# Optimization experiments

Measured on AMD Instinct MI355X. Metric: run time of the kernel, lower is better.

The kernel has to match this reference:

```python
import jax, jax.numpy as jnp
import numpy as np

N, D, C = 32768, 1024, 256
GAMMA = 1e-4


def setup_inputs() -> dict:
    key = jax.random.key(0)
    kx, kw = jax.random.split(key)
    X = jax.random.normal(kx, (N, D), dtype=jnp.float32)
    # lcls linear params: weight [C, D], bias [C] (torch nn.Linear layout)
    W = jax.random.normal(kw, (C, D), dtype=jnp.float32) * (1.0 / np.sqrt(D))
    b = jnp.zeros((C,), dtype=jnp.float32)
    return {"X": X, "W": W, "b": b}


def reference(X, W, b):
    # P = softmax(X @ W.T + b) over cluster dim C
    P = jax.nn.softmax(X @ W.T + b, axis=-1)            # [N, C]
    # Reorder P @ P.T @ X -> P @ (P.T @ X): avoids the O(N^2) affinity matrix
    PtX = jnp.einsum('nc,nd->cd', P, X)                  # [C, D]
    return X + GAMMA * (P @ PtX)                         # [N, D]
```

## Files before the change

kernel.cpp:

```cpp
#include <hip/hip_runtime.h>
#include <hip/hip_bf16.h>
#include <stdint.h>

#define N_TOK 32768
#define DIM   1024
#define NC    256
#define GAMMA_F 1e-4f

typedef unsigned short u16;
typedef __attribute__((ext_vector_type(8))) short bf16x8;
typedef __attribute__((ext_vector_type(4))) float f32x4;

__device__ __forceinline__ u16 f2b(float f) {
  union { float f; uint32_t u; } c; c.f = f;
  uint32_t u = c.u;
  return (u16)((u + 0x7FFFu + ((u >> 16) & 1u)) >> 16);
}

__device__ __forceinline__ void gll16(const void* g, void* l) {
  __builtin_amdgcn_global_load_lds(
      (const __attribute__((address_space(1))) unsigned int*)g,
      (__attribute__((address_space(3))) unsigned int*)l, 16, 0, 0);
}

__global__ __launch_bounds__(256) void k0_transpose(const float* __restrict__ X,
                                                    u16* __restrict__ TX) {
  __shared__ u16 tile[64][68];
  const int n0 = blockIdx.x * 64;
  const int d0 = blockIdx.y * 64;
  const int t = threadIdx.x;
  const int r = t >> 4;
  const int c4 = (t & 15) * 4;
#pragma unroll
  for (int i = 0; i < 4; ++i) {
    const int row = r + i * 16;
    const float4 v = *reinterpret_cast<const float4*>(&X[(size_t)(n0 + row) * DIM + d0 + c4]);
    tile[row][c4 + 0] = f2b(v.x);
    tile[row][c4 + 1] = f2b(v.y);
    tile[row][c4 + 2] = f2b(v.z);
    tile[row][c4 + 3] = f2b(v.w);
  }
  __syncthreads();
#pragma unroll
  for (int i = 0; i < 4; ++i) {
    const int drow = r + i * 16;
    ushort4 o;
    o.x = tile[c4 + 0][drow];
    o.y = tile[c4 + 1][drow];
    o.z = tile[c4 + 2][drow];
    o.w = tile[c4 + 3][drow];
    *reinterpret_cast<ushort4*>(&TX[(size_t)(d0 + drow) * N_TOK + n0 + c4]) = o;
  }
}

__global__ __launch_bounds__(256) void k0_convert_w(const float* __restrict__ W,
                                                    u16* __restrict__ Wb) {
  const int idx = (blockIdx.x * 256 + threadIdx.x) * 4;
  const float4 v = *reinterpret_cast<const float4*>(&W[idx]);
  ushort4 o;
  o.x = f2b(v.x); o.y = f2b(v.y); o.z = f2b(v.z); o.w = f2b(v.w);
  *reinterpret_cast<ushort4*>(&Wb[idx]) = o;
}

__global__ __launch_bounds__(256, 3) void p1_gemm(const float* __restrict__ X,
                                                  const u16* __restrict__ Wb,
                                                  float* __restrict__ S) {
  __shared__ u16 As[128 * 64];
  __shared__ u16 Bs[128 * 64];
  const int t = threadIdx.x;
  const int lane = t & 63, wave = t >> 6;
  const int wm = wave & 1, wn = wave >> 1;
  const int n0 = blockIdx.x * 128;
  const int c0 = blockIdx.y * 128;
  const int frow = lane & 15, fk = (lane >> 4) * 8;
  const int sr = t >> 3, sc = (t & 7) * 8;
  const int laneoff = lane * 8;
  f32x4 acc[4][4] = {};
  for (int kt = 0; kt < 16; ++kt) {
    const int k0 = kt * 64;
#pragma unroll
    for (int p = 0; p < 4; ++p) {
      const int row = sr + p * 32;
      const float4 v0 = *reinterpret_cast<const float4*>(&X[(size_t)(n0 + row) * DIM + k0 + sc]);
      const float4 v1 = *reinterpret_cast<const float4*>(&X[(size_t)(n0 + row) * DIM + k0 + sc + 4]);
      bf16x8 u;
      u[0] = (short)f2b(v0.x); u[1] = (short)f2b(v0.y);
      u[2] = (short)f2b(v0.z); u[3] = (short)f2b(v0.w);
      u[4] = (short)f2b(v1.x); u[5] = (short)f2b(v1.y);
      u[6] = (short)f2b(v1.z); u[7] = (short)f2b(v1.w);
      *reinterpret_cast<bf16x8*>(&As[row * 64 + sc]) = u;
    }
#pragma unroll
    for (int i = 0; i < 4; ++i) {
      const int e = (wave * 4 + i) * 512;
      const int brow = (e + laneoff) >> 6;
      const int bcol = (e + laneoff) & 63;
      gll16(&Wb[(size_t)(c0 + brow) * DIM + k0 + bcol], &Bs[e]);
    }
    __syncthreads();
#pragma unroll
    for (int ks = 0; ks < 2; ++ks) {
      bf16x8 af[4], bg[4];
#pragma unroll
      for (int m = 0; m < 4; ++m)
        af[m] = *reinterpret_cast<const bf16x8*>(&As[(wm * 64 + m * 16 + frow) * 64 + ks * 32 + fk]);
#pragma unroll
      for (int n = 0; n < 4; ++n)
        bg[n] = *reinterpret_cast<const bf16x8*>(&Bs[(wn * 64 + n * 16 + frow) * 64 + ks * 32 + fk]);
#pragma unroll
      for (int m = 0; m < 4; ++m)
#pragma unroll
        for (int n = 0; n < 4; ++n)
          acc[m][n] = __builtin_amdgcn_mfma_f32_16x16x32_bf16(af[m], bg[n], acc[m][n], 0, 0, 0);
    }
    __syncthreads();
  }
#pragma unroll
  for (int m = 0; m < 4; ++m) {
    const int row = wm * 64 + m * 16 + (lane >> 4) * 4;
#pragma unroll
    for (int n = 0; n < 4; ++n) {
      const int col = wn * 64 + n * 16 + frow;
#pragma unroll
      for (int j = 0; j < 4; ++j)
        S[(size_t)(n0 + row + j) * NC + c0 + col] = acc[m][n][j];
    }
  }
}

__global__ __launch_bounds__(256) void k1_softmax(const float* __restrict__ S,
                                                  const float* __restrict__ bias,
                                                  u16* __restrict__ P,
                                                  u16* __restrict__ PT) {
  __shared__ u16 T[64][256];
  const int t = threadIdx.x;
  const int w = t >> 6, lane = t & 63;
  const int n0 = blockIdx.x * 64;
  const int col = lane * 4;
  const float4 bv = *reinterpret_cast<const float4*>(&bias[col]);
#pragma unroll
  for (int i = 0; i < 16; ++i) {
    const int row = i * 4 + w;
    float4 v = *reinterpret_cast<const float4*>(&S[(size_t)(n0 + row) * NC + col]);
    v.x += bv.x; v.y += bv.y; v.z += bv.z; v.w += bv.w;
    float mx = fmaxf(fmaxf(v.x, v.y), fmaxf(v.z, v.w));
    for (int s = 1; s < 64; s <<= 1) mx = fmaxf(mx, __shfl_xor(mx, s, 64));
    const float k = 1.44269504088896f;
    const float e0 = exp2f((v.x - mx) * k), e1 = exp2f((v.y - mx) * k);
    const float e2 = exp2f((v.z - mx) * k), e3 = exp2f((v.w - mx) * k);
    float sm = e0 + e1 + e2 + e3;
    for (int s = 1; s < 64; s <<= 1) sm += __shfl_xor(sm, s, 64);
    const float inv = 1.0f / sm;
    ushort4 o;
    o.x = f2b(e0 * inv); o.y = f2b(e1 * inv); o.z = f2b(e2 * inv); o.w = f2b(e3 * inv);
    *reinterpret_cast<ushort4*>(&P[(size_t)(n0 + row) * NC + col]) = o;
    *reinterpret_cast<ushort4*>(&T[row][col]) = o;
  }
  __syncthreads();
  const int c = t;
#pragma unroll
  for (int g = 0; g < 16; ++g) {
    ushort4 o;
    o.x = T[g * 4 + 0][c];
    o.y = T[g * 4 + 1][c];
    o.z = T[g * 4 + 2][c];
    o.w = T[g * 4 + 3][c];
    *reinterpret_cast<ushort4*>(&PT[(size_t)c * N_TOK + n0 + g * 4]) = o;
  }
}

__global__ __launch_bounds__(256, 3) void p2_gemm(const u16* __restrict__ TX,
                                                  const u16* __restrict__ PT,
                                                  float* __restrict__ part) {
  __shared__ u16 As[128 * 64];
  __shared__ u16 Bs[128 * 64];
  const int t = threadIdx.x;
  const int lane = t & 63, wave = t >> 6;
  const int wm = wave & 1, wn = wave >> 1;
  const int sk = blockIdx.x;
  const int d0 = (blockIdx.y >> 1) * 128;
  const int c0 = (blockIdx.y & 1) * 128;
  const int frow = lane & 15, fk = (lane >> 4) * 8;
  const int laneoff = lane * 8;
  f32x4 acc[4][4] = {};
  for (int kt = 0; kt < 16; ++kt) {
    const size_t k0 = (size_t)sk * 1024 + kt * 64;
#pragma unroll
    for (int i = 0; i < 4; ++i) {
      const int e = (wave * 4 + i) * 512;
      const int brow = (e + laneoff) >> 6;
      const int bcol = (e + laneoff) & 63;
      gll16(&TX[(size_t)(d0 + brow) * N_TOK + k0 + bcol], &As[e]);
      gll16(&PT[(size_t)(c0 + brow) * N_TOK + k0 + bcol], &Bs[e]);
    }
    __syncthreads();
#pragma unroll
    for (int ks = 0; ks < 2; ++ks) {
      bf16x8 af[4], bg[4];
#pragma unroll
      for (int m = 0; m < 4; ++m)
        af[m] = *reinterpret_cast<const bf16x8*>(&As[(wm * 64 + m * 16 + frow) * 64 + ks * 32 + fk]);
#pragma unroll
      for (int n = 0; n < 4; ++n)
        bg[n] = *reinterpret_cast<const bf16x8*>(&Bs[(wn * 64 + n * 16 + frow) * 64 + ks * 32 + fk]);
#pragma unroll
      for (int m = 0; m < 4; ++m)
#pragma unroll
        for (int n = 0; n < 4; ++n)
          acc[m][n] = __builtin_amdgcn_mfma_f32_16x16x32_bf16(af[m], bg[n], acc[m][n], 0, 0, 0);
    }
    __syncthreads();
  }
  float* pl = part + (size_t)sk * (DIM * NC);
#pragma unroll
  for (int m = 0; m < 4; ++m) {
    const int row = wm * 64 + m * 16 + (lane >> 4) * 4;
#pragma unroll
    for (int n = 0; n < 4; ++n) {
      const int colc = wn * 64 + n * 16 + frow;
#pragma unroll
      for (int j = 0; j < 4; ++j)
        pl[(size_t)(d0 + row + j) * NC + c0 + colc] = acc[m][n][j];
    }
  }
}

__global__ __launch_bounds__(256) void k2_reduce(const float* __restrict__ part,
                                                 u16* __restrict__ PtXb) {
  const int g = (blockIdx.x * 256 + threadIdx.x) * 4;
  f32x4 s = {0.f, 0.f, 0.f, 0.f};
#pragma unroll
  for (int p = 0; p < 32; ++p)
    s += *reinterpret_cast<const f32x4*>(&part[(size_t)p * (DIM * NC) + g]);
  ushort4 o;
  o.x = f2b(s[0] * GAMMA_F); o.y = f2b(s[1] * GAMMA_F);
  o.z = f2b(s[2] * GAMMA_F); o.w = f2b(s[3] * GAMMA_F);
  *reinterpret_cast<ushort4*>(&PtXb[g]) = o;
}

__global__ __launch_bounds__(256, 3) void p3_gemm(const u16* __restrict__ P,
                                                  const u16* __restrict__ PtXb,
                                                  const float* __restrict__ X,
                                                  float* __restrict__ Out) {
  __shared__ u16 As[128 * 64];
  __shared__ u16 Bs[128 * 64];
  const int t = threadIdx.x;
  const int lane = t & 63, wave = t >> 6;
  const int wm = wave & 1, wn = wave >> 1;
  const int n0 = blockIdx.x * 128;
  const int d0 = blockIdx.y * 128;
  const int frow = lane & 15, fk = (lane >> 4) * 8;
  const int laneoff = lane * 8;
  f32x4 acc[4][4] = {};
  for (int kt = 0; kt < 4; ++kt) {
    const int k0 = kt * 64;
#pragma unroll
    for (int i = 0; i < 4; ++i) {
      const int e = (wave * 4 + i) * 512;
      const int brow = (e + laneoff) >> 6;
      const int bcol = (e + laneoff) & 63;
      gll16(&P[(size_t)(n0 + brow) * NC + k0 + bcol], &As[e]);
      gll16(&PtXb[(size_t)(d0 + brow) * NC + k0 + bcol], &Bs[e]);
    }
    __syncthreads();
#pragma unroll
    for (int ks = 0; ks < 2; ++ks) {
      bf16x8 af[4], bg[4];
#pragma unroll
      for (int m = 0; m < 4; ++m)
        af[m] = *reinterpret_cast<const bf16x8*>(&As[(wm * 64 + m * 16 + frow) * 64 + ks * 32 + fk]);
#pragma unroll
      for (int n = 0; n < 4; ++n)
        bg[n] = *reinterpret_cast<const bf16x8*>(&Bs[(wn * 64 + n * 16 + frow) * 64 + ks * 32 + fk]);
#pragma unroll
      for (int m = 0; m < 4; ++m)
#pragma unroll
        for (int n = 0; n < 4; ++n)
          acc[m][n] = __builtin_amdgcn_mfma_f32_16x16x32_bf16(af[m], bg[n], acc[m][n], 0, 0, 0);
    }
    __syncthreads();
  }
#pragma unroll
  for (int m = 0; m < 4; ++m) {
    const int row = wm * 64 + m * 16 + (lane >> 4) * 4;
#pragma unroll
    for (int n = 0; n < 4; ++n) {
      const int colc = wn * 64 + n * 16 + frow;
#pragma unroll
      for (int j = 0; j < 4; ++j) {
        const size_t off = (size_t)(n0 + row + j) * DIM + d0 + colc;
        Out[off] = X[off] + acc[m][n][j];
      }
    }
  }
}

extern "C" void kernel_launch(void* const* d_in, const int* in_sizes, int n_in,
                              void* d_out, int out_size, void* d_ws, size_t ws_size,
                              hipStream_t stream) {
  const float* X = (const float*)d_in[0];
  const float* W = (const float*)d_in[1];
  const float* b = (const float*)d_in[2];
  float* Out = (float*)d_out;
  char* ws = (char*)d_ws;

  const size_t OFF_TX   = 0;
  const size_t OFF_WB   = (size_t)64 << 20;
  const size_t OFF_PTXB = OFF_WB + ((size_t)512 << 10);
  const size_t OFF_S    = (size_t)65 << 20;
  const size_t OFF_P    = (size_t)97 << 20;
  const size_t OFF_PT   = (size_t)113 << 20;
  const size_t NEED     = (size_t)129 << 20;
  if (ws_size < NEED) return;

  u16*   TX   = (u16*)(ws + OFF_TX);
  u16*   Wb   = (u16*)(ws + OFF_WB);
  u16*   PtXb = (u16*)(ws + OFF_PTXB);
  float* S    = (float*)(ws + OFF_S);
  float* part = S;
  u16*   Pp   = (u16*)(ws + OFF_P);
  u16*   PT   = (u16*)(ws + OFF_PT);

  k0_transpose<<<dim3(N_TOK / 64, DIM / 64), 256, 0, stream>>>(X, TX);
  k0_convert_w<<<dim3((NC * DIM) / 1024), 256, 0, stream>>>(W, Wb);
  p1_gemm<<<dim3(N_TOK / 128, NC / 128), 256, 0, stream>>>(X, Wb, S);
  k1_softmax<<<dim3(N_TOK / 64), 256, 0, stream>>>(S, b, Pp, PT);
  p2_gemm<<<dim3(32, 16), 256, 0, stream>>>(TX, PT, part);
  k2_reduce<<<dim3((DIM * NC) / 1024), 256, 0, stream>>>(part, PtXb);
  p3_gemm<<<dim3(N_TOK / 128, DIM / 128), 256, 0, stream>>>(Pp, PtXb, X, Out);
}
```

Before: 439.6 us.

## Fuse logits GEMM with softmax, swizzle LDS tiles, stage epilogues through LDS

The first GEMM and the softmax become one kernel. Each block now computes a full 64x256 logit tile, applies bias and softmax from shared memory, and writes P and its transpose directly. This removes the fp32 S round trip through global memory and one kernel launch. All three GEMMs also get XOR-swizzled LDS layouts to reduce bank conflicts. The p2 and p3 epilogues are staged through LDS so stores are coalesced float4 writes. The cost is a larger LDS footprint, with occupancy dropping from 3 to 2 blocks per CU.

```diff
diff --git a/kernel.cpp b/kernel.cpp
--- a/kernel.cpp
+++ b/kernel.cpp
@@ -22,6 +22,7 @@
       (const __attribute__((address_space(1))) unsigned int*)g,
       (__attribute__((address_space(3))) unsigned int*)l, 16, 0, 0);
 }
+
 
 __global__ __launch_bounds__(256) void k0_transpose(const float* __restrict__ X,
                                                     u16* __restrict__ TX) {
@@ -62,147 +63,158 @@
   *reinterpret_cast<ushort4*>(&Wb[idx]) = o;
 }
 
-__global__ __launch_bounds__(256, 3) void p1_gemm(const float* __restrict__ X,
-                                                  const u16* __restrict__ Wb,
-                                                  float* __restrict__ S) {
-  __shared__ u16 As[128 * 64];
-  __shared__ u16 Bs[128 * 64];
+__global__ __launch_bounds__(256, 2) void p1_fused(const float* __restrict__ X,
+                                                   const u16* __restrict__ Wb,
+                                                   const float* __restrict__ bias,
+                                                   u16* __restrict__ P,
+                                                   u16* __restrict__ PT) {
+  __shared__ __align__(16) char smem[66560];
+  u16* As = (u16*)smem;
+  u16* Bs = (u16*)(smem + 8192);
   const int t = threadIdx.x;
   const int lane = t & 63, wave = t >> 6;
   const int wm = wave & 1, wn = wave >> 1;
-  const int n0 = blockIdx.x * 128;
-  const int c0 = blockIdx.y * 128;
-  const int frow = lane & 15, fk = (lane >> 4) * 8;
-  const int sr = t >> 3, sc = (t & 7) * 8;
-  const int laneoff = lane * 8;
-  f32x4 acc[4][4] = {};
+  const int n0 = blockIdx.x * 64;
+  const int frow = lane & 15, fq = lane >> 4;
+  const int au = t & 7, ar0 = t >> 3;
+  const int bug = (lane & 7) ^ (lane >> 3);
+
+  f32x4 acc[2][8] = {};
   for (int kt = 0; kt < 16; ++kt) {
     const int k0 = kt * 64;
 #pragma unroll
-    for (int p = 0; p < 4; ++p) {
-      const int row = sr + p * 32;
-      const float4 v0 = *reinterpret_cast<const float4*>(&X[(size_t)(n0 + row) * DIM + k0 + sc]);
-      const float4 v1 = *reinterpret_cast<const float4*>(&X[(size_t)(n0 + row) * DIM + k0 + sc + 4]);
+    for (int h = 0; h < 2; ++h) {
+      const int r = ar0 + h * 32;
+      const size_t gb = (size_t)(n0 + r) * DIM + k0 + au * 8;
+      const float4 v0 = *reinterpret_cast<const float4*>(&X[gb]);
+      const float4 v1 = *reinterpret_cast<const float4*>(&X[gb + 4]);
       bf16x8 u;
       u[0] = (short)f2b(v0.x); u[1] = (short)f2b(v0.y);
       u[2] = (short)f2b(v0.z); u[3] = (short)f2b(v0.w);
       u[4] = (short)f2b(v1.x); u[5] = (short)f2b(v1.y);
       u[6] = (short)f2b(v1.z); u[7] = (short)f2b(v1.w);
-      *reinterpret_cast<bf16x8*>(&As[row * 64 + sc]) = u;
-    }
-#pragma unroll
-    for (int i = 0; i < 4; ++i) {
-      const int e = (wave * 4 + i) * 512;
-      const int brow = (e + laneoff) >> 6;
-      const int bcol = (e + laneoff) & 63;
-      gll16(&Wb[(size_t)(c0 + brow) * DIM + k0 + bcol], &Bs[e]);
+      *reinterpret_cast<bf16x8*>(&As[r * 64 + ((au ^ (r & 7)) * 8)]) = u;
+    }
+#pragma unroll
+    for (int i = 0; i < 8; ++i) {
+      const int chunk = wave * 8 + i;
+      const int brow = chunk * 8 + (lane >> 3);
+      gll16(&Wb[(size_t)brow * DIM + k0 + bug * 8], &Bs[chunk * 512]);
     }
     __syncthreads();
 #pragma unroll
     for (int ks = 0; ks < 2; ++ks) {
-      bf16x8 af[4], bg[4];
-#pragma unroll
-      for (int m = 0; m < 4; ++m)
-        af[m] = *reinterpret_cast<const bf16x8*>(&As[(wm * 64 + m * 16 + frow) * 64 + ks * 32 + fk]);
-#pragma unroll
-      for (int n = 0; n < 4; ++n)
-        bg[n] = *reinterpret_cast<const bf16x8*>(&Bs[(wn * 64 + n * 16 + frow) * 64 + ks * 32 + fk]);
-#pragma unroll
-      for (int m = 0; m < 4; ++m)
-#pragma unroll
-        for (int n = 0; n < 4; ++n)
+      bf16x8 af[2], bg[8];
+#pragma unroll
+      for (int m = 0; m < 2; ++m) {
+        const int r = wm * 32 + m * 16 + frow;
+        af[m] = *reinterpret_cast<const bf16x8*>(&As[r * 64 + (((ks * 4 + fq) ^ (r & 7)) * 8)]);
+      }
+#pragma unroll
+      for (int n = 0; n < 8; ++n) {
+        const int r = wn * 128 + n * 16 + frow;
+        bg[n] = *reinterpret_cast<const bf16x8*>(&Bs[r * 64 + (((ks * 4 + fq) ^ (r & 7)) * 8)]);
+      }
+#pragma unroll
+      for (int m = 0; m < 2; ++m)
+#pragma unroll
+        for (int n = 0; n < 8; ++n)
           acc[m][n] = __builtin_amdgcn_mfma_f32_16x16x32_bf16(af[m], bg[n], acc[m][n], 0, 0, 0);
     }
     __syncthreads();
   }
-#pragma unroll
-  for (int m = 0; m < 4; ++m) {
-    const int row = wm * 64 + m * 16 + (lane >> 4) * 4;
-#pragma unroll
-    for (int n = 0; n < 4; ++n) {
-      const int col = wn * 64 + n * 16 + frow;
+  float* Sf = (float*)smem;
+#pragma unroll
+  for (int m = 0; m < 2; ++m)
+#pragma unroll
+    for (int n = 0; n < 8; ++n) {
+      const int row = wm * 32 + m * 16 + fq * 4;
+      const int col = wn * 128 + n * 16 + frow;
 #pragma unroll
       for (int j = 0; j < 4; ++j)
-        S[(size_t)(n0 + row + j) * NC + c0 + col] = acc[m][n][j];
-    }
-  }
-}
-
-__global__ __launch_bounds__(256) void k1_softmax(const float* __restrict__ S,
-                                                  const float* __restrict__ bias,
-                                                  u16* __restrict__ P,
-                                                  u16* __restrict__ PT) {
-  __shared__ u16 T[64][256];
-  const int t = threadIdx.x;
-  const int w = t >> 6, lane = t & 63;
-  const int n0 = blockIdx.x * 64;
-  const int col = lane * 4;
-  const float4 bv = *reinterpret_cast<const float4*>(&bias[col]);
+        Sf[(row + j) * 260 + col] = acc[m][n][j];
+    }
+  __syncthreads();
+  u16* Su = (u16*)smem;
+  const float4 bv = *reinterpret_cast<const float4*>(&bias[lane * 4]);
+  const float l2e = 1.44269504088896f;
 #pragma unroll
   for (int i = 0; i < 16; ++i) {
-    const int row = i * 4 + w;
-    float4 v = *reinterpret_cast<const float4*>(&S[(size_t)(n0 + row) * NC + col]);
+    const int row = wave * 16 + i;
+    float4 v = *reinterpret_cast<const float4*>(&Sf[row * 260 + lane * 4]);
     v.x += bv.x; v.y += bv.y; v.z += bv.z; v.w += bv.w;
     float mx = fmaxf(fmaxf(v.x, v.y), fmaxf(v.z, v.w));
+#pragma unroll
     for (int s = 1; s < 64; s <<= 1) mx = fmaxf(mx, __shfl_xor(mx, s, 64));
-    const float k = 1.44269504088896f;
-    const float e0 = exp2f((v.x - mx) * k), e1 = exp2f((v.y - mx) * k);
-    const float e2 = exp2f((v.z - mx) * k), e3 = exp2f((v.w - mx) * k);
+    const float e0 = exp2f((v.x - mx) * l2e), e1 = exp2f((v.y - mx) * l2e);
+    const float e2 = exp2f((v.z - mx) * l2e), e3 = exp2f((v.w - mx) * l2e);
     float sm = e0 + e1 + e2 + e3;
+#pragma unroll
     for (int s = 1; s < 64; s <<= 1) sm += __shfl_xor(sm, s, 64);
     const float inv = 1.0f / sm;
     ushort4 o;
-    o.x = f2b(e0 * inv); o.y = f2b(e1 * inv); o.z = f2b(e2 * inv); o.w = f2b(e3 * inv);
-    *reinterpret_cast<ushort4*>(&P[(size_t)(n0 + row) * NC + col]) = o;
-    *reinterpret_cast<ushort4*>(&T[row][col]) = o;
-  }
-  __syncthreads();
-  const int c = t;
-#pragma unroll
-  for (int g = 0; g < 16; ++g) {
+    o.x = f2b(e0 * inv); o.y = f2b(e1 * inv);
+    o.z = f2b(e2 * inv); o.w = f2b(e3 * inv);
+    *reinterpret_cast<ushort4*>(&P[(size_t)(n0 + row) * NC + lane * 4]) = o;
+    const int rb = row & 31;
+    Su[row * 520 + (((lane * 4 + 0) ^ rb)) * 2] = o.x;
+    Su[row * 520 + (((lane * 4 + 1) ^ rb)) * 2] = o.y;
+    Su[row * 520 + (((lane * 4 + 2) ^ rb)) * 2] = o.z;
+    Su[row * 520 + (((lane * 4 + 3) ^ rb)) * 2] = o.w;
+  }
+  __syncthreads();
+#pragma unroll
+  for (int it = 0; it < 16; ++it) {
+    const int c = it * 16 + wave * 4 + fq;
+    const int n = frow * 4;
     ushort4 o;
-    o.x = T[g * 4 + 0][c];
-    o.y = T[g * 4 + 1][c];
-    o.z = T[g * 4 + 2][c];
-    o.w = T[g * 4 + 3][c];
-    *reinterpret_cast<ushort4*>(&PT[(size_t)c * N_TOK + n0 + g * 4]) = o;
-  }
-}
-
-__global__ __launch_bounds__(256, 3) void p2_gemm(const u16* __restrict__ TX,
+    o.x = Su[(n + 0) * 520 + ((c ^ ((n + 0) & 31))) * 2];
+    o.y = Su[(n + 1) * 520 + ((c ^ ((n + 1) & 31))) * 2];
+    o.z = Su[(n + 2) * 520 + ((c ^ ((n + 2) & 31))) * 2];
+    o.w = Su[(n + 3) * 520 + ((c ^ ((n + 3) & 31))) * 2];
+    *reinterpret_cast<ushort4*>(&PT[(size_t)c * N_TOK + n0 + n]) = o;
+  }
+}
+
+__global__ __launch_bounds__(256, 2) void p2_gemm(const u16* __restrict__ TX,
                                                   const u16* __restrict__ PT,
                                                   float* __restrict__ part) {
-  __shared__ u16 As[128 * 64];
-  __shared__ u16 Bs[128 * 64];
+  __shared__ __align__(16) char smem[67584];
+  u16* As = (u16*)smem;
+  u16* Bs = (u16*)(smem + 16384);
   const int t = threadIdx.x;
   const int lane = t & 63, wave = t >> 6;
   const int wm = wave & 1, wn = wave >> 1;
   const int sk = blockIdx.x;
   const int d0 = (blockIdx.y >> 1) * 128;
   const int c0 = (blockIdx.y & 1) * 128;
-  const int frow = lane & 15, fk = (lane >> 4) * 8;
-  const int laneoff = lane * 8;
+  const int frow = lane & 15, fq = lane >> 4;
+  const int srow = lane >> 3;
+  const int bug = (lane & 7) ^ (lane >> 3);
   f32x4 acc[4][4] = {};
   for (int kt = 0; kt < 16; ++kt) {
     const size_t k0 = (size_t)sk * 1024 + kt * 64;
 #pragma unroll
     for (int i = 0; i < 4; ++i) {
-      const int e = (wave * 4 + i) * 512;
-      const int brow = (e + laneoff) >> 6;
-      const int bcol = (e + laneoff) & 63;
-      gll16(&TX[(size_t)(d0 + brow) * N_TOK + k0 + bcol], &As[e]);
-      gll16(&PT[(size_t)(c0 + brow) * N_TOK + k0 + bcol], &Bs[e]);
+      const int chunk = wave * 4 + i;
+      const int r = chunk * 8 + srow;
+      gll16(&TX[(size_t)(d0 + r) * N_TOK + k0 + bug * 8], &As[chunk * 512]);
+      gll16(&PT[(size_t)(c0 + r) * N_TOK + k0 + bug * 8], &Bs[chunk * 512]);
     }
     __syncthreads();
 #pragma unroll
     for (int ks = 0; ks < 2; ++ks) {
       bf16x8 af[4], bg[4];
 #pragma unroll
-      for (int m = 0; m < 4; ++m)
-        af[m] = *reinterpret_cast<const bf16x8*>(&As[(wm * 64 + m * 16 + frow) * 64 + ks * 32 + fk]);
-#pragma unroll
-      for (int n = 0; n < 4; ++n)
-        bg[n] = *reinterpret_cast<const bf16x8*>(&Bs[(wn * 64 + n * 16 + frow) * 64 + ks * 32 + fk]);
+      for (int m = 0; m < 4; ++m) {
+        const int r = wm * 64 + m * 16 + frow;
+        af[m] = *reinterpret_cast<const bf16x8*>(&As[r * 64 + (((ks * 4 + fq) ^ (r & 7)) * 8)]);
+      }
+#pragma unroll
+      for (int n = 0; n < 4; ++n) {
+        const int r = wn * 64 + n * 16 + frow;
+        bg[n] = *reinterpret_cast<const bf16x8*>(&Bs[r * 64 + (((ks * 4 + fq) ^ (r & 7)) * 8)]);
+      }
 #pragma unroll
       for (int m = 0; m < 4; ++m)
 #pragma unroll
@@ -211,17 +223,26 @@
     }
     __syncthreads();
   }
+  float* Cf = (float*)smem;
+#pragma unroll
+  for (int m = 0; m < 4; ++m)
+#pragma unroll
+    for (int n = 0; n < 4; ++n) {
+      const int row = wm * 64 + m * 16 + fq * 4;
+      const int col = wn * 64 + n * 16 + frow;
+#pragma unroll
+      for (int j = 0; j < 4; ++j)
+        Cf[(row + j) * 132 + col] = acc[m][n][j];
+    }
+  __syncthreads();
   float* pl = part + (size_t)sk * (DIM * NC);
-#pragma unroll
-  for (int m = 0; m < 4; ++m) {
-    const int row = wm * 64 + m * 16 + (lane >> 4) * 4;
-#pragma unroll
-    for (int n = 0; n < 4; ++n) {
-      const int colc = wn * 64 + n * 16 + frow;
-#pragma unroll
-      for (int j = 0; j < 4; ++j)
-        pl[(size_t)(d0 + row + j) * NC + c0 + colc] = acc[m][n][j];
-    }
+  const int cl = (t & 31) * 4;
+  const int rr = t >> 5;
+#pragma unroll
+  for (int p = 0; p < 16; ++p) {
+    const int row = p * 8 + rr;
+    const float4 v = *reinterpret_cast<const float4*>(&Cf[row * 132 + cl]);
+    *reinterpret_cast<float4*>(&pl[(size_t)(d0 + row) * NC + c0 + cl]) = v;
   }
 }
 
@@ -238,40 +259,45 @@
   *reinterpret_cast<ushort4*>(&PtXb[g]) = o;
 }
 
-__global__ __launch_bounds__(256, 3) void p3_gemm(const u16* __restrict__ P,
+__global__ __launch_bounds__(256, 2) void p3_gemm(const u16* __restrict__ P,
                                                   const u16* __restrict__ PtXb,
                                                   const float* __restrict__ X,
                                                   float* __restrict__ Out) {
-  __shared__ u16 As[128 * 64];
-  __shared__ u16 Bs[128 * 64];
+  __shared__ __align__(16) char smem[67584];
+  u16* As = (u16*)smem;
+  u16* Bs = (u16*)(smem + 16384);
   const int t = threadIdx.x;
   const int lane = t & 63, wave = t >> 6;
   const int wm = wave & 1, wn = wave >> 1;
   const int n0 = blockIdx.x * 128;
   const int d0 = blockIdx.y * 128;
-  const int frow = lane & 15, fk = (lane >> 4) * 8;
-  const int laneoff = lane * 8;
+  const int frow = lane & 15, fq = lane >> 4;
+  const int srow = lane >> 3;
+  const int bug = (lane & 7) ^ (lane >> 3);
   f32x4 acc[4][4] = {};
   for (int kt = 0; kt < 4; ++kt) {
     const int k0 = kt * 64;
 #pragma unroll
     for (int i = 0; i < 4; ++i) {
-      const int e = (wave * 4 + i) * 512;
-      const int brow = (e + laneoff) >> 6;
-      const int bcol = (e + laneoff) & 63;
-      gll16(&P[(size_t)(n0 + brow) * NC + k0 + bcol], &As[e]);
-      gll16(&PtXb[(size_t)(d0 + brow) * NC + k0 + bcol], &Bs[e]);
+      const int chunk = wave * 4 + i;
+      const int r = chunk * 8 + srow;
+      gll16(&P[(size_t)(n0 + r) * NC + k0 + bug * 8], &As[chunk * 512]);
+      gll16(&PtXb[(size_t)(d0 + r) * NC + k0 + bug * 8], &Bs[chunk * 512]);
     }
     __syncthreads();
 #pragma unroll
     for (int ks = 0; ks < 2; ++ks) {
       bf16x8 af[4], bg[4];
 #pragma unroll
-      for (int m = 0; m < 4; ++m)
-        af[m] = *reinterpret_cast<const bf16x8*>(&As[(wm * 64 + m * 16 + frow) * 64 + ks * 32 + fk]);
-#pragma unroll
-      for (int n = 0; n < 4; ++n)
-        bg[n] = *reinterpret_cast<const bf16x8*>(&Bs[(wn * 64 + n * 16 + frow) * 64 + ks * 32 + fk]);
+      for (int m = 0; m < 4; ++m) {
+        const int r = wm * 64 + m * 16 + frow;
+        af[m] = *reinterpret_cast<const bf16x8*>(&As[r * 64 + (((ks * 4 + fq) ^ (r & 7)) * 8)]);
+      }
+#pragma unroll
+      for (int n = 0; n < 4; ++n) {
+        const int r = wn * 64 + n * 16 + frow;
+        bg[n] = *reinterpret_cast<const bf16x8*>(&Bs[r * 64 + (((ks * 4 + fq) ^ (r & 7)) * 8)]);
+      }
 #pragma unroll
       for (int m = 0; m < 4; ++m)
 #pragma unroll
@@ -280,18 +306,28 @@
     }
     __syncthreads();
   }
-#pragma unroll
-  for (int m = 0; m < 4; ++m) {
-    const int row = wm * 64 + m * 16 + (lane >> 4) * 4;
+  float* Cf = (float*)smem;
+#pragma unroll
+  for (int m = 0; m < 4; ++m)
 #pragma unroll
     for (int n = 0; n < 4; ++n) {
-      const int colc = wn * 64 + n * 16 + frow;
-#pragma unroll
-      for (int j = 0; j < 4; ++j) {
-        const size_t off = (size_t)(n0 + row + j) * DIM + d0 + colc;
-        Out[off] = X[off] + acc[m][n][j];
-      }
-    }
+      const int row = wm * 64 + m * 16 + fq * 4;
+      const int col = wn * 64 + n * 16 + frow;
+#pragma unroll
+      for (int j = 0; j < 4; ++j)
+        Cf[(row + j) * 132 + col] = acc[m][n][j];
+    }
+  __syncthreads();
+  const int cl = (t & 31) * 4;
+  const int rr = t >> 5;
+#pragma unroll
+  for (int p = 0; p < 16; ++p) {
+    const int row = p * 8 + rr;
+    float4 v = *reinterpret_cast<const float4*>(&Cf[row * 132 + cl]);
+    const size_t off = (size_t)(n0 + row) * DIM + d0 + cl;
+    const float4 x = *reinterpret_cast<const float4*>(&X[off]);
+    v.x += x.x; v.y += x.y; v.z += x.z; v.w += x.w;
+    *reinterpret_cast<float4*>(&Out[off]) = v;
   }
 }
 
@@ -307,7 +343,7 @@
   const size_t OFF_TX   = 0;
   const size_t OFF_WB   = (size_t)64 << 20;
   const size_t OFF_PTXB = OFF_WB + ((size_t)512 << 10);
-  const size_t OFF_S    = (size_t)65 << 20;
+  const size_t OFF_PART = (size_t)65 << 20;
   const size_t OFF_P    = (size_t)97 << 20;
   const size_t OFF_PT   = (size_t)113 << 20;
   const size_t NEED     = (size_t)129 << 20;
@@ -316,15 +352,13 @@
   u16*   TX   = (u16*)(ws + OFF_TX);
   u16*   Wb   = (u16*)(ws + OFF_WB);
   u16*   PtXb = (u16*)(ws + OFF_PTXB);
-  float* S    = (float*)(ws + OFF_S);
-  float* part = S;
+  float* part = (float*)(ws + OFF_PART);
   u16*   Pp   = (u16*)(ws + OFF_P);
   u16*   PT   = (u16*)(ws + OFF_PT);
 
   k0_transpose<<<dim3(N_TOK / 64, DIM / 64), 256, 0, stream>>>(X, TX);
   k0_convert_w<<<dim3((NC * DIM) / 1024), 256, 0, stream>>>(W, Wb);
-  p1_gemm<<<dim3(N_TOK / 128, NC / 128), 256, 0, stream>>>(X, Wb, S);
-  k1_softmax<<<dim3(N_TOK / 64), 256, 0, stream>>>(S, b, Pp, PT);
+  p1_fused<<<dim3(N_TOK / 64), 256, 0, stream>>>(X, Wb, b, Pp, PT);
   p2_gemm<<<dim3(32, 16), 256, 0, stream>>>(TX, PT, part);
   k2_reduce<<<dim3((DIM * NC) / 1024), 256, 0, stream>>>(part, PtXb);
   p3_gemm<<<dim3(N_TOK / 128, DIM / 128), 256, 0, stream>>>(Pp, PtXb, X, Out);
```

Measured after the change: 378.4 us. 1.16x faster.
